# Kernel optimization log

Hardware: AMD Instinct MI355X
Metric: run time of the kernel (lower is better)

The kernel has to match this reference:

```python
import jax, jax.numpy as jnp
import numpy as np

BLK = 128          # quantization block size (group_shape = (1,128) act, (128,128) weight)
FP8_MAX = 448.0    # max finite value of float8_e4m3fn
EPS = 1e-6         # RMSNorm epsilon


def _rms_norm(x, weight):
    # RMSNorm: x / sqrt(mean(x^2) + eps) * weight
    var = jnp.mean(x * x, axis=-1, keepdims=True)
    return x * jax.lax.rsqrt(var + EPS) * weight


def _quant_dequant_act(x):
    # Per-token-group (1, BLK) dynamic FP8 quantization, then dequant (fake-quant).
    M, K = x.shape
    g = x.reshape(M, K // BLK, BLK)
    scale = jnp.maximum(jnp.max(jnp.abs(g), axis=-1, keepdims=True) / FP8_MAX, 1e-10)
    q = jnp.clip(g / scale, -FP8_MAX, FP8_MAX)
    q = q.astype(jnp.float8_e4m3fn).astype(jnp.float32)
    return (q * scale).reshape(M, K)


def _dequant_weight(w_fp8, ws):
    # w_fp8: [N, K] fp8-rounded values in fp32; ws: [N//BLK, K//BLK] block scales.
    s_full = jnp.repeat(jnp.repeat(ws, BLK, axis=0), BLK, axis=1)  # [N, K]
    return w_fp8 * s_full


def setup_inputs() -> dict:
    key = jax.random.key(0)
    k1, k2, k3, k4 = jax.random.split(key, 4)
    T, H = 4096, 4096
    x = jax.random.normal(k1, (T, H), dtype=jnp.float32)
    norm_w = jax.random.uniform(k2, (4, H), dtype=jnp.float32)
    w = jax.random.uniform(k3, (3, H, H), dtype=jnp.float32)
    wscale = jax.random.uniform(k4, (3, H // BLK, H // BLK), dtype=jnp.float32)
    return {"x": x, "norm_w": norm_w, "w": w, "wscale": wscale}


def reference(x, norm_w, w, wscale):
    # Weights are stored as FP8 in the original model (torch.rand(...).to(FP8_DTYPE)).
    w_fp8 = w.astype(jnp.float8_e4m3fn).astype(jnp.float32)  # [3, H, H]

    x = jax.nn.relu(x)
    resid = x
    # norm[0]: plain RMSNorm
    y = _rms_norm(x, norm_w[0])
    for i in range(3):
        # block-FP8 linear: quantize activation, dequantize weight, out = a @ W^T
        a = _quant_dequant_act(y)                    # [T, H]
        wd = _dequant_weight(w_fp8[i], wscale[i])    # [H, H]
        xi = a @ wd.T                                # [T, H]
        # fused add + RMSNorm: resid = xi + resid; y = rmsnorm(resid)
        resid = xi + resid
        y = _rms_norm(resid, norm_w[i + 1])
    return y
```

## Files before the change

### kernel.cpp

```cpp
#include <hip/hip_runtime.h>

typedef float f32x4 __attribute__((ext_vector_type(4)));
typedef int i32x4 __attribute__((ext_vector_type(4)));
typedef int i32x8 __attribute__((ext_vector_type(8)));

#define HDIM 4096
#define NKB 32

__global__ __launch_bounds__(256) void wquant_kernel(const float* __restrict__ w,
                                                     unsigned char* __restrict__ w8,
                                                     int n4) {
  int i = blockIdx.x * 256 + threadIdx.x;
  if (i >= n4) return;
  const float4 v = ((const float4*)w)[i];
  int p = 0;
  p = __builtin_amdgcn_cvt_pk_fp8_f32(v.x, v.y, p, false);
  p = __builtin_amdgcn_cvt_pk_fp8_f32(v.z, v.w, p, true);
  ((int*)w8)[i] = p;
}

template <int MODE>
__global__ __launch_bounds__(256) void norm_quant_kernel(
    const float* __restrict__ src, float* __restrict__ resid,
    const float* __restrict__ nw, unsigned char* __restrict__ qa,
    float* __restrict__ ascT, float* __restrict__ out) {
  const int row = blockIdx.x;
  const int tid = threadIdx.x;
  const float* srow = src + (size_t)row * HDIM;
  float4 v[4];
  float ss = 0.f;
#pragma unroll
  for (int c = 0; c < 4; ++c) {
    float4 t = ((const float4*)srow)[c * 256 + tid];
    if (MODE == 0) {
      t.x = fmaxf(t.x, 0.f); t.y = fmaxf(t.y, 0.f);
      t.z = fmaxf(t.z, 0.f); t.w = fmaxf(t.w, 0.f);
      ((float4*)(resid + (size_t)row * HDIM))[c * 256 + tid] = t;
    }
    v[c] = t;
    ss += t.x * t.x + t.y * t.y + t.z * t.z + t.w * t.w;
  }
#pragma unroll
  for (int m = 32; m >= 1; m >>= 1) ss += __shfl_xor(ss, m);
  __shared__ float red[4];
  if ((tid & 63) == 0) red[tid >> 6] = ss;
  __syncthreads();
  const float tot = red[0] + red[1] + red[2] + red[3];
  const float rstd = rsqrtf(tot * (1.f / (float)HDIM) + 1e-6f);
#pragma unroll
  for (int c = 0; c < 4; ++c) {
    float4 wv = ((const float4*)nw)[c * 256 + tid];
    float4 y;
    y.x = v[c].x * rstd * wv.x;
    y.y = v[c].y * rstd * wv.y;
    y.z = v[c].z * rstd * wv.z;
    y.w = v[c].w * rstd * wv.w;
    if (MODE == 2) {
      ((float4*)(out + (size_t)row * HDIM))[c * 256 + tid] = y;
    } else {
      float amax = fmaxf(fmaxf(fabsf(y.x), fabsf(y.y)), fmaxf(fabsf(y.z), fabsf(y.w)));
#pragma unroll
      for (int m = 16; m >= 1; m >>= 1) amax = fmaxf(amax, __shfl_xor(amax, m));
      const float scale = fmaxf(amax / 448.f, 1e-10f);
      const float qinv = __builtin_amdgcn_rcpf(scale);
      float qx = fminf(fmaxf(y.x * qinv, -448.f), 448.f);
      float qy = fminf(fmaxf(y.y * qinv, -448.f), 448.f);
      float qz = fminf(fmaxf(y.z * qinv, -448.f), 448.f);
      float qw = fminf(fmaxf(y.w * qinv, -448.f), 448.f);
      int p = 0;
      p = __builtin_amdgcn_cvt_pk_fp8_f32(qx, qy, p, false);
      p = __builtin_amdgcn_cvt_pk_fp8_f32(qz, qw, p, true);
      const int off = (c * 256 + tid) << 2;
      *(int*)(qa + (size_t)row * HDIM + off) = p;
      if ((tid & 31) == 0) ascT[(c * 8 + (tid >> 5)) * HDIM + row] = scale;
    }
  }
}

__global__ __launch_bounds__(512, 2) void gemm256_kernel(
    const unsigned char* __restrict__ qa, const float* __restrict__ ascT,
    const unsigned char* __restrict__ w8, const float* __restrict__ wsc,
    float* __restrict__ resid) {
  extern __shared__ char smem[];
  char* ldsA = smem;
  char* ldsB = smem + 65536;
  char* ldsS = smem + 131072;

  const int tid = threadIdx.x;
  const int lane = tid & 63;
  const int wid = tid >> 6;
  const int wm = wid >> 1;
  const int wn = wid & 1;

  const int bflat = blockIdx.y * 16 + blockIdx.x;
  const int bswz = (bflat & 7) * 32 + (bflat >> 3);
  const int m0 = (bswz >> 4) << 8;
  const int n0 = (bswz & 15) << 8;

  const int ln15 = lane & 15;
  const int g = lane >> 4;

  int ofs[4];
  {
    const int rowp = ((tid >> 7) & 3) * 16 + (tid & 15);
    const int kp = ((tid >> 4) & 3) * 32 + ((tid >> 6) & 1) * 16;
#pragma unroll
    for (int ch = 0; ch < 4; ++ch) ofs[ch] = (ch * 64 + rowp) * HDIM + kp;
  }
  const unsigned char* gA = qa + (size_t)m0 * HDIM;
  const unsigned char* gB = w8 + (size_t)n0 * HDIM;
  const float* sS = ascT + m0 + lane * 4;

  const int nb = __builtin_amdgcn_readfirstlane((n0 >> 7) + wn);
  const float* wsp = wsc + nb * NKB;

  const int abase = wm * 8192 + lane * 16;
  const int bbase = wn * 16384 + lane * 16;
  const int svb = wm * 256 + g * 16;

  f32x4 acc[4][8];
#pragma unroll
  for (int i = 0; i < 4; ++i)
#pragma unroll
    for (int j = 0; j < 8; ++j) acc[i][j] = (f32x4){0.f, 0.f, 0.f, 0.f};

  i32x8 aF[4];
  i32x8 bFa[2];
  i32x8 bFb[2];
  f32x4 svw[4];

#define STAGE_A(CH, KB, BUF)                                                              \
  __builtin_amdgcn_global_load_lds(                                                       \
      (const __attribute__((address_space(1))) void*)(gA + ofs[CH] + (KB)*128),           \
      (__attribute__((address_space(3))) void*)(ldsA + (BUF)*32768 + (CH)*8192 + tid*16), \
      16, 0, 0)
#define STAGE_B(CH, KB, BUF)                                                              \
  __builtin_amdgcn_global_load_lds(                                                       \
      (const __attribute__((address_space(1))) void*)(gB + ofs[CH] + (KB)*128),           \
      (__attribute__((address_space(3))) void*)(ldsB + (BUF)*32768 + (CH)*8192 + tid*16), \
      16, 0, 0)
#define STAGE_S(KB, BUF)                                                                  \
  __builtin_amdgcn_global_load_lds(                                                       \
      (const __attribute__((address_space(1))) void*)(sS + (size_t)(KB)*HDIM),            \
      (__attribute__((address_space(3))) void*)(ldsS + (BUF)*1024 + lane*16), 16, 0, 0)

#define RD_A(MT)                                                                          \
  {                                                                                       \
    const char* pA_ = ldsA + cb + abase + (MT)*2048;                                      \
    i32x4 lo_ = *(const i32x4*)pA_;                                                       \
    i32x4 hi_ = *(const i32x4*)(pA_ + 1024);                                              \
    aF[MT] = __builtin_shufflevector(lo_, hi_, 0, 1, 2, 3, 4, 5, 6, 7);                   \
  }
#define RD_SVW(MT) svw[MT] = *(const f32x4*)(ldsS + cur * 1024 + svb + (MT)*64) * sw;
#define RD_BS(BS, NH)                                                                     \
  {                                                                                       \
    const char* p0_ = ldsB + cb + bbase + ((NH)*2) * 2048;                                \
    i32x4 l0_ = *(const i32x4*)p0_;                                                       \
    i32x4 h0_ = *(const i32x4*)(p0_ + 1024);                                              \
    BS[0] = __builtin_shufflevector(l0_, h0_, 0, 1, 2, 3, 4, 5, 6, 7);                    \
    const char* p1_ = p0_ + 2048;                                                         \
    i32x4 l1_ = *(const i32x4*)p1_;                                                       \
    i32x4 h1_ = *(const i32x4*)(p1_ + 1024);                                              \
    BS[1] = __builtin_shufflevector(l1_, h1_, 0, 1, 2, 3, 4, 5, 6, 7);                    \
  }

#define PH_WAIT                                                                           \
  asm volatile("s_waitcnt lgkmcnt(0)" ::: "memory");                                      \
  __builtin_amdgcn_sched_barrier(0);

#define MFMA_PH(MTA, MTB, NH, BS)                                                         \
  __builtin_amdgcn_s_setprio(1);                                                          \
  {                                                                                       \
    const f32x4 z_ = (f32x4){0.f, 0.f, 0.f, 0.f};                                         \
    f32x4 t0 = __builtin_amdgcn_mfma_scale_f32_16x16x128_f8f6f4(                          \
        aF[MTA], BS[0], z_, 0, 0, 0, 127, 0, 127);                                        \
    f32x4 t1 = __builtin_amdgcn_mfma_scale_f32_16x16x128_f8f6f4(                          \
        aF[MTA], BS[1], z_, 0, 0, 0, 127, 0, 127);                                        \
    f32x4 t2 = __builtin_amdgcn_mfma_scale_f32_16x16x128_f8f6f4(                          \
        aF[MTB], BS[0], z_, 0, 0, 0, 127, 0, 127);                                        \
    f32x4 t3 = __builtin_amdgcn_mfma_scale_f32_16x16x128_f8f6f4(                          \
        aF[MTB], BS[1], z_, 0, 0, 0, 127, 0, 127);                                        \
    __builtin_amdgcn_s_setprio(0);                                                        \
    acc[MTA][(NH)*2]     += t0 * svw[MTA];                                                \
    acc[MTA][(NH)*2 + 1] += t1 * svw[MTA];                                                \
    acc[MTB][(NH)*2]     += t2 * svw[MTB];                                                \
    acc[MTB][(NH)*2 + 1] += t3 * svw[MTB];                                                \
  }

  STAGE_S(0, 0); STAGE_A(0, 0, 0); STAGE_A(1, 0, 0); STAGE_A(2, 0, 0); STAGE_A(3, 0, 0);
  STAGE_B(0, 0, 0); STAGE_B(2, 0, 0); STAGE_B(1, 0, 0); STAGE_B(3, 0, 0);
  asm volatile("s_waitcnt vmcnt(2)" ::: "memory");
  __builtin_amdgcn_s_barrier();

#pragma unroll 2
  for (int kb = 0; kb < NKB; ++kb) {
    const int cur = kb & 1;
    const int nxt = cur ^ 1;
    const int kbn = (kb + 1) & (NKB - 1);
    const int cb = cur * 32768;
    const float sw = wsp[kb];
    RD_A(0) RD_A(1) RD_SVW(0) RD_SVW(1) RD_BS(bFa, 0)
    STAGE_S(kbn, nxt); STAGE_A(0, kbn, nxt);
    PH_WAIT MFMA_PH(0, 1, 0, bFa)
    RD_A(2) RD_A(3) RD_SVW(2) RD_SVW(3)
    STAGE_A(1, kbn, nxt); STAGE_A(2, kbn, nxt);
    PH_WAIT MFMA_PH(2, 3, 0, bFa)
    RD_BS(bFb, 1)
    STAGE_A(3, kbn, nxt); STAGE_B(0, kbn, nxt);
    PH_WAIT MFMA_PH(2, 3, 1, bFb)
    PH_WAIT MFMA_PH(0, 1, 1, bFb)
    asm volatile("s_waitcnt vmcnt(6)" ::: "memory");
    __builtin_amdgcn_s_barrier();
    RD_BS(bFa, 2)
    STAGE_B(2, kbn, nxt);
    PH_WAIT MFMA_PH(0, 1, 2, bFa)
    STAGE_B(1, kbn, nxt);
    PH_WAIT MFMA_PH(2, 3, 2, bFa)
    RD_BS(bFb, 3)
    STAGE_B(3, kbn, nxt);
    PH_WAIT MFMA_PH(2, 3, 3, bFb)
    PH_WAIT MFMA_PH(0, 1, 3, bFb)
    asm volatile("s_waitcnt vmcnt(2)" ::: "memory");
    __builtin_amdgcn_s_barrier();
  }

  const size_t rowstart = (size_t)(m0 + wm * 64 + g * 4) * HDIM + n0 + wn * 128 + ln15;
#pragma unroll
  for (int mt = 0; mt < 4; ++mt)
#pragma unroll
    for (int ntg = 0; ntg < 8; ++ntg)
#pragma unroll
      for (int j = 0; j < 4; ++j) {
        const size_t idx = rowstart + (size_t)(mt * 16 + j) * HDIM + ntg * 16;
        resid[idx] += acc[mt][ntg][j];
      }
#undef MFMA_PH
#undef PH_WAIT
#undef RD_BS
#undef RD_SVW
#undef RD_A
#undef STAGE_A
#undef STAGE_B
#undef STAGE_S
}

extern "C" void kernel_launch(void* const* d_in, const int* in_sizes, int n_in,
                              void* d_out, int out_size, void* d_ws, size_t ws_size,
                              hipStream_t stream) {
  const float* x = (const float*)d_in[0];
  const float* norm_w = (const float*)d_in[1];
  const float* w = (const float*)d_in[2];
  const float* wscale = (const float*)d_in[3];
  float* out = (float*)d_out;
  char* ws = (char*)d_ws;

  size_t off = 0;
  unsigned char* w8 = (unsigned char*)(ws + off); off += 3ull * HDIM * HDIM;
  float* resid = (float*)(ws + off);              off += (size_t)HDIM * HDIM * 4;
  unsigned char* qa = (unsigned char*)(ws + off); off += (size_t)HDIM * HDIM;
  float* asc = (float*)(ws + off);                off += (size_t)NKB * HDIM * 4;

  hipFuncSetAttribute((const void*)gemm256_kernel,
                      hipFuncAttributeMaxDynamicSharedMemorySize, 133120);

  const int n4 = 3 * HDIM * HDIM / 4;
  wquant_kernel<<<n4 / 256, 256, 0, stream>>>(w, w8, n4);
  norm_quant_kernel<0><<<HDIM, 256, 0, stream>>>(x, resid, norm_w, qa, asc, nullptr);
  for (int i = 0; i < 3; ++i) {
    gemm256_kernel<<<dim3(16, 16), 512, 133120, stream>>>(
        qa, asc, w8 + (size_t)i * HDIM * HDIM, wscale + i * NKB * NKB, resid);
    if (i < 2)
      norm_quant_kernel<1><<<HDIM, 256, 0, stream>>>(resid, nullptr, norm_w + (size_t)(i + 1) * HDIM, qa, asc, nullptr);
    else
      norm_quant_kernel<2><<<HDIM, 256, 0, stream>>>(resid, nullptr, norm_w + (size_t)3 * HDIM, nullptr, nullptr, out);
  }
}
```

Measured before the change: 400.7 us.

## Load A fragments directly from global memory instead of staging through LDS

The GEMM no longer stages the activation tile through shared memory. Each wave now loads its A fragments straight from global memory into registers at the start of every k-block, which halves LDS use and drops the A-side LDS writes and reads. The B and scale pipeline is re-timed with new vmcnt values and extra sched_barriers. The cost is that A loads are no longer shared: the two waves that share the same rows each fetch them from global or L2, and the load latency is exposed at the start of each iteration with no prefetch.

```diff
diff --git a/kernel.cpp b/kernel.cpp
--- a/kernel.cpp
+++ b/kernel.cpp
@@ -82,9 +82,8 @@
     const unsigned char* __restrict__ w8, const float* __restrict__ wsc,
     float* __restrict__ resid) {
   extern __shared__ char smem[];
-  char* ldsA = smem;
-  char* ldsB = smem + 65536;
-  char* ldsS = smem + 131072;
+  char* ldsB = smem;
+  char* ldsS = smem + 65536;
 
   const int tid = threadIdx.x;
   const int lane = tid & 63;
@@ -107,14 +106,15 @@
 #pragma unroll
     for (int ch = 0; ch < 4; ++ch) ofs[ch] = (ch * 64 + rowp) * HDIM + kp;
   }
-  const unsigned char* gA = qa + (size_t)m0 * HDIM;
   const unsigned char* gB = w8 + (size_t)n0 * HDIM;
   const float* sS = ascT + m0 + lane * 4;
 
+  const unsigned char* gAl =
+      qa + (size_t)(m0 + wm * 64 + ln15) * HDIM + g * 32;
+
   const int nb = __builtin_amdgcn_readfirstlane((n0 >> 7) + wn);
   const float* wsp = wsc + nb * NKB;
 
-  const int abase = wm * 8192 + lane * 16;
   const int bbase = wn * 16384 + lane * 16;
   const int svb = wm * 256 + g * 16;
 
@@ -129,11 +129,6 @@
   i32x8 bFb[2];
   f32x4 svw[4];
 
-#define STAGE_A(CH, KB, BUF)                                                              \
-  __builtin_amdgcn_global_load_lds(                                                       \
-      (const __attribute__((address_space(1))) void*)(gA + ofs[CH] + (KB)*128),           \
-      (__attribute__((address_space(3))) void*)(ldsA + (BUF)*32768 + (CH)*8192 + tid*16), \
-      16, 0, 0)
 #define STAGE_B(CH, KB, BUF)                                                              \
   __builtin_amdgcn_global_load_lds(                                                       \
       (const __attribute__((address_space(1))) void*)(gB + ofs[CH] + (KB)*128),           \
@@ -146,9 +141,9 @@
 
 #define RD_A(MT)                                                                          \
   {                                                                                       \
-    const char* pA_ = ldsA + cb + abase + (MT)*2048;                                      \
+    const unsigned char* pA_ = gAl + (size_t)(MT)*16 * HDIM + kb * 128;                   \
     i32x4 lo_ = *(const i32x4*)pA_;                                                       \
-    i32x4 hi_ = *(const i32x4*)(pA_ + 1024);                                              \
+    i32x4 hi_ = *(const i32x4*)(pA_ + 16);                                                \
     aF[MT] = __builtin_shufflevector(lo_, hi_, 0, 1, 2, 3, 4, 5, 6, 7);                   \
   }
 #define RD_SVW(MT) svw[MT] = *(const f32x4*)(ldsS + cur * 1024 + svb + (MT)*64) * sw;
@@ -187,10 +182,10 @@
     acc[MTB][(NH)*2 + 1] += t3 * svw[MTB];                                                \
   }
 
-  STAGE_S(0, 0); STAGE_A(0, 0, 0); STAGE_A(1, 0, 0); STAGE_A(2, 0, 0); STAGE_A(3, 0, 0);
-  STAGE_B(0, 0, 0); STAGE_B(2, 0, 0); STAGE_B(1, 0, 0); STAGE_B(3, 0, 0);
+  STAGE_S(0, 0); STAGE_B(0, 0, 0); STAGE_B(2, 0, 0); STAGE_B(1, 0, 0); STAGE_B(3, 0, 0);
   asm volatile("s_waitcnt vmcnt(2)" ::: "memory");
   __builtin_amdgcn_s_barrier();
+  __builtin_amdgcn_sched_barrier(0);
 
 #pragma unroll 2
   for (int kb = 0; kb < NKB; ++kb) {
@@ -199,22 +194,22 @@
     const int kbn = (kb + 1) & (NKB - 1);
     const int cb = cur * 32768;
     const float sw = wsp[kb];
-    RD_A(0) RD_A(1) RD_SVW(0) RD_SVW(1) RD_BS(bFa, 0)
-    STAGE_S(kbn, nxt); STAGE_A(0, kbn, nxt);
+    RD_A(0) RD_A(1) RD_A(2) RD_A(3)
+    RD_SVW(0) RD_SVW(1) RD_BS(bFa, 0)
+    STAGE_S(kbn, nxt); STAGE_B(0, kbn, nxt);
     PH_WAIT MFMA_PH(0, 1, 0, bFa)
-    RD_A(2) RD_A(3) RD_SVW(2) RD_SVW(3)
-    STAGE_A(1, kbn, nxt); STAGE_A(2, kbn, nxt);
+    RD_SVW(2) RD_SVW(3)
     PH_WAIT MFMA_PH(2, 3, 0, bFa)
     RD_BS(bFb, 1)
-    STAGE_A(3, kbn, nxt); STAGE_B(0, kbn, nxt);
+    STAGE_B(2, kbn, nxt);
     PH_WAIT MFMA_PH(2, 3, 1, bFb)
     PH_WAIT MFMA_PH(0, 1, 1, bFb)
-    asm volatile("s_waitcnt vmcnt(6)" ::: "memory");
+    asm volatile("s_waitcnt vmcnt(3)" ::: "memory");
     __builtin_amdgcn_s_barrier();
+    __builtin_amdgcn_sched_barrier(0);
     RD_BS(bFa, 2)
-    STAGE_B(2, kbn, nxt);
+    STAGE_B(1, kbn, nxt);
     PH_WAIT MFMA_PH(0, 1, 2, bFa)
-    STAGE_B(1, kbn, nxt);
     PH_WAIT MFMA_PH(2, 3, 2, bFa)
     RD_BS(bFb, 3)
     STAGE_B(3, kbn, nxt);
@@ -222,6 +217,7 @@
     PH_WAIT MFMA_PH(0, 1, 3, bFb)
     asm volatile("s_waitcnt vmcnt(2)" ::: "memory");
     __builtin_amdgcn_s_barrier();
+    __builtin_amdgcn_sched_barrier(0);
   }
 
   const size_t rowstart = (size_t)(m0 + wm * 64 + g * 4) * HDIM + n0 + wn * 128 + ln15;
@@ -239,7 +235,6 @@
 #undef RD_BS
 #undef RD_SVW
 #undef RD_A
-#undef STAGE_A
 #undef STAGE_B
 #undef STAGE_S
 }
@@ -261,13 +256,13 @@
   float* asc = (float*)(ws + off);                off += (size_t)NKB * HDIM * 4;
 
   hipFuncSetAttribute((const void*)gemm256_kernel,
-                      hipFuncAttributeMaxDynamicSharedMemorySize, 133120);
+                      hipFuncAttributeMaxDynamicSharedMemorySize, 67584);
 
   const int n4 = 3 * HDIM * HDIM / 4;
   wquant_kernel<<<n4 / 256, 256, 0, stream>>>(w, w8, n4);
   norm_quant_kernel<0><<<HDIM, 256, 0, stream>>>(x, resid, norm_w, qa, asc, nullptr);
   for (int i = 0; i < 3; ++i) {
-    gemm256_kernel<<<dim3(16, 16), 512, 133120, stream>>>(
+    gemm256_kernel<<<dim3(16, 16), 512, 67584, stream>>>(
         qa, asc, w8 + (size_t)i * HDIM * HDIM, wscale + i * NKB * NKB, resid);
     if (i < 2)
       norm_quant_kernel<1><<<HDIM, 256, 0, stream>>>(resid, nullptr, norm_w + (size_t)(i + 1) * HDIM, qa, asc, nullptr);
```

New measurement: 534.7 us. 33.4% more time.
